# Kernel tuning notes

Measured on AMD Instinct MI355X. Metric: run time of the kernel, lower is better.

The kernel has to match this reference:

```python
import jax, jax.numpy as jnp
import numpy as np

EPS = 1e-7
MAX_NORM = 1.0 - 1e-3  # projection radius of the unit Poincare ball (c=1)
ALPHA = 0.2            # LeakyReLU negative slope
NEG_INF = -9e15


def _proj(x, max_norm=MAX_NORM):
    # Project points back inside the Poincare ball along the last dim.
    norm = jnp.clip(jnp.linalg.norm(x, axis=-1, keepdims=True), EPS)
    return jnp.where(norm > max_norm, x / norm * max_norm, x)


def _logmap0(x):
    # Log map at the origin of the Poincare ball, c = 1.
    norm = jnp.clip(jnp.linalg.norm(x, axis=-1, keepdims=True), EPS, 1.0 - EPS)
    return jnp.arctanh(norm) * x / norm


def _expmap0(v):
    # Exp map at the origin of the Poincare ball, c = 1.
    norm = jnp.clip(jnp.linalg.norm(v, axis=-1, keepdims=True), EPS)
    return jnp.tanh(norm) * v / norm


def setup_inputs() -> dict:
    key = jax.random.key(0)
    k1, k2, k3 = jax.random.split(key, 3)
    N, D = 12288, 128
    # points strictly inside the ball: ||x|| ~ 0.01*sqrt(128) ~ 0.11 < 1
    x = jax.random.normal(k1, (N, D), dtype=jnp.float32) * 0.01
    adj = jax.random.randint(k2, (N, N), 0, 2, dtype=jnp.int32)
    # attention vector a, as in init: N(0, 0.2) then proj(a, 0.9) row-wise
    a = jax.random.normal(k3, (2 * D, 1), dtype=jnp.float32) * 0.2
    a = _proj(a, 0.9)
    return {"x": x, "adj": adj, "a": a}


def reference(x, adj, a):
    D = a.shape[0] // 2
    x_tan = _logmap0(x)                       # [N, D]
    wh1 = x_tan @ a[:D]                       # [N, 1]
    wh2 = x_tan @ a[D:]                       # [N, 1]
    e = jax.nn.leaky_relu(wh1 + wh2.T, ALPHA)  # [N, N] additive scores
    scores = jnp.where(adj > 0, e, NEG_INF)
    attention = jax.nn.softmax(scores, axis=1)  # dropout omitted (eval mode)
    x_tan_prime = attention @ x_tan            # [N, D]
    return _proj(_expmap0(x_tan_prime))
```

## Files before the change

kernel.cpp:

```cpp
#include <hip/hip_runtime.h>
#include <math.h>

#define NN 12288
#define DD 128
#define EPSF 1e-7f
#define MAXNORM (1.0f - 1e-3f)
#define CSPLIT 4
#define CCOLS (NN / CSPLIT)
#define CSTEPS (CCOLS / 128)

typedef __attribute__((ext_vector_type(8))) short short8_t;
typedef __attribute__((ext_vector_type(4))) float float4_t;
typedef unsigned short ushort_t;

__device__ __forceinline__ unsigned short f2bf(float f) {
    unsigned int u = __builtin_bit_cast(unsigned int, f);
    unsigned int r = u + 0x7FFFu + ((u >> 16) & 1u);
    return (unsigned short)(r >> 16);
}

__global__ __launch_bounds__(128) void prep_kernel(
    const float* __restrict__ x, const float* __restrict__ a,
    ushort_t* __restrict__ xtb,
    float* __restrict__ wh1, float* __restrict__ wh2)
{
    const int r = blockIdx.x;
    const int t = threadIdx.x;
    const float xv = x[r * DD + t];
    const float a1 = a[t];
    const float a2 = a[DD + t];
    float s0 = xv * xv, s1 = xv * a1, s2 = xv * a2;
    #pragma unroll
    for (int o = 32; o > 0; o >>= 1) {
        s0 += __shfl_xor(s0, o);
        s1 += __shfl_xor(s1, o);
        s2 += __shfl_xor(s2, o);
    }
    __shared__ float red[6];
    const int w = t >> 6;
    if ((t & 63) == 0) { red[w * 3 + 0] = s0; red[w * 3 + 1] = s1; red[w * 3 + 2] = s2; }
    __syncthreads();
    const float sumsq = red[0] + red[3];
    const float d1    = red[1] + red[4];
    const float d2    = red[2] + red[5];
    const float nraw  = sqrtf(sumsq);
    const float nrm   = fminf(fmaxf(nraw, EPSF), 1.0f - EPSF);
    const float scale = atanhf(nrm) / nrm;
    xtb[(size_t)r * DD + t] = f2bf(xv * scale);
    if (t == 0) {
        wh1[r] = scale * d1;
        wh2[r] = scale * d2;
    }
}

__global__ __launch_bounds__(256) void swizzle_kernel(
    const ushort_t* __restrict__ xtb, ushort_t* __restrict__ xtB)
{
    __shared__ ushort_t raw[32 * 136];
    const int C = blockIdx.x;
    const int t = threadIdx.x;
    #pragma unroll
    for (int p = 0; p < 2; ++p) {
        const int idx = p * 256 + t;
        const int j = idx >> 4, cell = idx & 15;
        const uint4 v = *(const uint4*)(xtb + (size_t)(C * 32 + j) * DD + cell * 8);
        *(uint4*)&raw[j * 136 + cell * 8] = v;
    }
    __syncthreads();
    #pragma unroll
    for (int p = 0; p < 2; ++p) {
        const int oc = p * 256 + t;
        const int dt = oc >> 6;
        const int l6 = oc & 63;
        const int l15 = l6 & 15, q = l6 >> 4;
        short8_t v;
        #pragma unroll
        for (int e = 0; e < 8; ++e)
            v[e] = (short)raw[(q * 8 + e) * 136 + dt * 16 + l15];
        *(short8_t*)(xtB + (size_t)C * 4096 + oc * 8) = v;
    }
}

__global__ __launch_bounds__(256, 2) void attn_kernel(
    const int* __restrict__ adj,
    const ushort_t* __restrict__ xtB,
    const float* __restrict__ wh1, const float* __restrict__ wh2,
    float* __restrict__ pout, float* __restrict__ plsum)
{
    __shared__ __align__(16) ushort_t Bl0[128 * DD];
    __shared__ __align__(16) ushort_t Bl1[128 * DD];
    __shared__ __align__(16) float wh2_lds[CCOLS];

    const int t = threadIdx.x;
    const int w = t >> 6, lane = t & 63;
    const int l15 = lane & 15, quad = lane >> 4;
    const int cy = blockIdx.y;
    const int jcol0 = cy * CCOLS;
    const int rowbase = blockIdx.x * 64 + w * 16;

    #pragma unroll
    for (int m = 0; m < CCOLS / 256; ++m)
        wh2_lds[m * 256 + t] = wh2[jcol0 + m * 256 + t];
    const float wh1i = wh1[rowbase + l15];

    const int* adj_lane = adj + (size_t)(rowbase + l15) * NN + jcol0 + quad * 8;
    const uint4* Bsrc = (const uint4*)(xtB + (size_t)(jcol0 >> 5) * 4096);

    float4_t acc[8];
    #pragma unroll
    for (int dt = 0; dt < 8; ++dt) acc[dt] = (float4_t)0.0f;
    float lsum = 0.0f;

    uint4 sr[8];
    int4 Aa[8], Ab[8];

    auto stage_load = [&](int st) {
        const uint4* sp = Bsrc + (size_t)st * 2048 + t;
        #pragma unroll
        for (int r = 0; r < 8; ++r) sr[r] = sp[r * 256];
    };
    auto stage_write = [&](ushort_t* buf) {
        uint4* d = (uint4*)buf + t;
        #pragma unroll
        for (int r = 0; r < 8; ++r) d[r * 256] = sr[r];
    };
    auto adj_load = [&](int st, int4 (&A)[8]) {
        const int* bp = adj_lane + st * 128;
        #pragma unroll
        for (int kc = 0; kc < 4; ++kc) {
            A[kc * 2 + 0] = *(const int4*)(bp + kc * 32);
            A[kc * 2 + 1] = *(const int4*)(bp + kc * 32 + 4);
        }
    };

    auto compute = [&](int st, const ushort_t* buf, const int4 (&A)[8]) {
        #pragma unroll
        for (int kc = 0; kc < 4; ++kc) {
            const int4 Av = A[kc * 2 + 0], Ac = A[kc * 2 + 1];
            const int wbase = st * 128 + kc * 32 + quad * 8;
            const float4 Wa = *(const float4*)&wh2_lds[wbase];
            const float4 Wb = *(const float4*)&wh2_lds[wbase + 4];
            const float u0 = wh1i + Wa.x, u1 = wh1i + Wa.y;
            const float u2 = wh1i + Wa.z, u3 = wh1i + Wa.w;
            const float u4 = wh1i + Wb.x, u5 = wh1i + Wb.y;
            const float u6 = wh1i + Wb.z, u7 = wh1i + Wb.w;
            const float p0 = (Av.x > 0) ? __expf(fmaxf(u0, 0.2f * u0)) : 0.0f;
            const float p1 = (Av.y > 0) ? __expf(fmaxf(u1, 0.2f * u1)) : 0.0f;
            const float p2 = (Av.z > 0) ? __expf(fmaxf(u2, 0.2f * u2)) : 0.0f;
            const float p3 = (Av.w > 0) ? __expf(fmaxf(u3, 0.2f * u3)) : 0.0f;
            const float p4 = (Ac.x > 0) ? __expf(fmaxf(u4, 0.2f * u4)) : 0.0f;
            const float p5 = (Ac.y > 0) ? __expf(fmaxf(u5, 0.2f * u5)) : 0.0f;
            const float p6 = (Ac.z > 0) ? __expf(fmaxf(u6, 0.2f * u6)) : 0.0f;
            const float p7 = (Ac.w > 0) ? __expf(fmaxf(u7, 0.2f * u7)) : 0.0f;
            lsum += ((p0 + p1) + (p2 + p3)) + ((p4 + p5) + (p6 + p7));
            short8_t af;
            af[0] = (short)f2bf(p0); af[1] = (short)f2bf(p1);
            af[2] = (short)f2bf(p2); af[3] = (short)f2bf(p3);
            af[4] = (short)f2bf(p4); af[5] = (short)f2bf(p5);
            af[6] = (short)f2bf(p6); af[7] = (short)f2bf(p7);
            const ushort_t* Bp = buf + kc * 4096 + lane * 8;
            #pragma unroll
            for (int dt = 0; dt < 8; ++dt) {
                const short8_t Bf = *(const short8_t*)(Bp + dt * 512);
                acc[dt] = __builtin_amdgcn_mfma_f32_16x16x32_bf16(af, Bf, acc[dt], 0, 0, 0);
            }
        }
    };

    stage_load(0);
    stage_write(Bl0);
    adj_load(0, Aa);
    __syncthreads();

    #pragma unroll 1
    for (int st0 = 0; st0 < CSTEPS; st0 += 2) {
        if (st0 + 1 < CSTEPS) { stage_load(st0 + 1); adj_load(st0 + 1, Ab); }
        compute(st0, Bl0, Aa);
        if (st0 + 1 < CSTEPS) stage_write(Bl1);
        __syncthreads();
        if (st0 + 1 >= CSTEPS) break;
        if (st0 + 2 < CSTEPS) { stage_load(st0 + 2); adj_load(st0 + 2, Aa); }
        compute(st0 + 1, Bl1, Ab);
        if (st0 + 2 < CSTEPS) stage_write(Bl0);
        __syncthreads();
    }

    float v = lsum;
    v += __shfl_xor(v, 16);
    v += __shfl_xor(v, 32);
    if (quad == 0) plsum[(size_t)cy * NN + rowbase + l15] = v;
    #pragma unroll
    for (int dt = 0; dt < 8; ++dt)
        #pragma unroll
        for (int reg = 0; reg < 4; ++reg)
            pout[((size_t)cy * NN + rowbase + quad * 4 + reg) * DD + dt * 16 + l15]
                = acc[dt][reg];
}

__global__ __launch_bounds__(128) void reduce_kernel(
    const float* __restrict__ pout, const float* __restrict__ plsum,
    float* __restrict__ out)
{
    const int i = blockIdx.x;
    const int t = threadIdx.x;
    float v = 0.0f;
    #pragma unroll
    for (int s = 0; s < CSPLIT; ++s) v += pout[((size_t)s * NN + i) * DD + t];
    float ls = 0.0f;
    #pragma unroll
    for (int s = 0; s < CSPLIT; ++s) ls += plsum[(size_t)s * NN + i];
    v /= ls;
    float ss = v * v;
    #pragma unroll
    for (int o = 1; o < 64; o <<= 1) ss += __shfl_xor(ss, o);
    __shared__ float r2[2];
    if ((t & 63) == 0) r2[t >> 6] = ss;
    __syncthreads();
    const float total = r2[0] + r2[1];
    const float nraw = sqrtf(total);
    const float nv   = fmaxf(nraw, EPSF);
    const float th   = tanhf(nv);
    const float ysc  = th / nv;
    const float nyr  = ysc * nraw;
    const float ny   = fmaxf(nyr, EPSF);
    const float psc  = (ny > MAXNORM) ? (MAXNORM / ny) : 1.0f;
    const float os   = ysc * psc;
    out[(size_t)i * DD + t] = v * os;
}

extern "C" void kernel_launch(void* const* d_in, const int* in_sizes, int n_in,
                              void* d_out, int out_size, void* d_ws, size_t ws_size,
                              hipStream_t stream) {
    const float* x   = (const float*)d_in[0];
    const int*   adj = (const int*)d_in[1];
    const float* a   = (const float*)d_in[2];
    float* out = (float*)d_out;

    char* ws = (char*)d_ws;
    ushort_t* xtb = (ushort_t*)ws;  ws += (size_t)NN * DD * sizeof(ushort_t);
    ushort_t* xtB = (ushort_t*)ws;  ws += (size_t)NN * DD * sizeof(ushort_t);
    float* wh1 = (float*)ws;        ws += NN * sizeof(float);
    float* wh2 = (float*)ws;        ws += NN * sizeof(float);
    float* plsum = (float*)ws;      ws += (size_t)CSPLIT * NN * sizeof(float);
    float* pout  = (float*)ws;

    prep_kernel<<<NN, 128, 0, stream>>>(x, a, xtb, wh1, wh2);
    swizzle_kernel<<<NN / 32, 256, 0, stream>>>(xtb, xtB);
    attn_kernel<<<dim3(NN / 64, CSPLIT), 256, 0, stream>>>(
        adj, xtB, wh1, wh2, pout, plsum);
    reduce_kernel<<<NN, 128, 0, stream>>>(pout, plsum, out);
}
```

Before: 951.4 us.

## Stage B tiles in 512-row slabs and triple-buffer adjacency loads

The attention kernel drops its double-buffered 128-row LDS stages and instead loads a 512-row slab of bf16 features into one 128 KB shared buffer. Each slab then feeds four compute steps with only two barriers per slab. Adjacency rows are now prefetched two steps ahead through three register buffers, with the loop fully unrolled so the buffer choice is resolved at compile time. The aim is fewer barriers and longer-latency hiding for the adjacency stream. In exchange, occupancy drops to one block per CU (launch bounds go from 2 to 1), and the slab load is no longer overlapped with compute, so each slab stalls on the full copy.

```diff
diff --git a/kernel.cpp b/kernel.cpp
--- a/kernel.cpp
+++ b/kernel.cpp
@@ -8,6 +8,7 @@
 #define CSPLIT 4
 #define CCOLS (NN / CSPLIT)
 #define CSTEPS (CCOLS / 128)
+#define SLABS (CSTEPS / 4)
 
 typedef __attribute__((ext_vector_type(8))) short short8_t;
 typedef __attribute__((ext_vector_type(4))) float float4_t;
@@ -81,14 +82,13 @@
     }
 }
 
-__global__ __launch_bounds__(256, 2) void attn_kernel(
+__global__ __launch_bounds__(256, 1) void attn_kernel(
     const int* __restrict__ adj,
     const ushort_t* __restrict__ xtB,
     const float* __restrict__ wh1, const float* __restrict__ wh2,
     float* __restrict__ pout, float* __restrict__ plsum)
 {
-    __shared__ __align__(16) ushort_t Bl0[128 * DD];
-    __shared__ __align__(16) ushort_t Bl1[128 * DD];
+    __shared__ __align__(16) ushort_t B_lds[512 * DD];
     __shared__ __align__(16) float wh2_lds[CCOLS];
 
     const int t = threadIdx.x;
@@ -111,19 +111,8 @@
     for (int dt = 0; dt < 8; ++dt) acc[dt] = (float4_t)0.0f;
     float lsum = 0.0f;
 
-    uint4 sr[8];
-    int4 Aa[8], Ab[8];
-
-    auto stage_load = [&](int st) {
-        const uint4* sp = Bsrc + (size_t)st * 2048 + t;
-        #pragma unroll
-        for (int r = 0; r < 8; ++r) sr[r] = sp[r * 256];
-    };
-    auto stage_write = [&](ushort_t* buf) {
-        uint4* d = (uint4*)buf + t;
-        #pragma unroll
-        for (int r = 0; r < 8; ++r) d[r * 256] = sr[r];
-    };
+    int4 A0[8], A1[8], A2[8];
+
     auto adj_load = [&](int st, int4 (&A)[8]) {
         const int* bp = adj_lane + st * 128;
         #pragma unroll
@@ -133,7 +122,29 @@
         }
     };
 
-    auto compute = [&](int st, const ushort_t* buf, const int4 (&A)[8]) {
+    auto stage = [&](int sl) {
+        const uint4* sp = Bsrc + (size_t)sl * 8192 + t;
+        uint4* d = (uint4*)B_lds + t;
+        uint4 sa[8], sb[8];
+        #pragma unroll
+        for (int m = 0; m < 8; ++m) sa[m] = sp[m * 256];
+        #pragma unroll
+        for (int m = 0; m < 8; ++m) sb[m] = sp[(8 + m) * 256];
+        #pragma unroll
+        for (int m = 0; m < 8; ++m) d[m * 256] = sa[m];
+        #pragma unroll
+        for (int m = 0; m < 8; ++m) sa[m] = sp[(16 + m) * 256];
+        #pragma unroll
+        for (int m = 0; m < 8; ++m) d[(8 + m) * 256] = sb[m];
+        #pragma unroll
+        for (int m = 0; m < 8; ++m) sb[m] = sp[(24 + m) * 256];
+        #pragma unroll
+        for (int m = 0; m < 8; ++m) d[(16 + m) * 256] = sa[m];
+        #pragma unroll
+        for (int m = 0; m < 8; ++m) d[(24 + m) * 256] = sb[m];
+    };
+
+    auto compute = [&](int st, const int4 (&A)[8]) {
         #pragma unroll
         for (int kc = 0; kc < 4; ++kc) {
             const int4 Av = A[kc * 2 + 0], Ac = A[kc * 2 + 1];
@@ -158,7 +169,7 @@
             af[2] = (short)f2bf(p2); af[3] = (short)f2bf(p3);
             af[4] = (short)f2bf(p4); af[5] = (short)f2bf(p5);
             af[6] = (short)f2bf(p6); af[7] = (short)f2bf(p7);
-            const ushort_t* Bp = buf + kc * 4096 + lane * 8;
+            const ushort_t* Bp = B_lds + ((st & 3) * 4 + kc) * 4096 + lane * 8;
             #pragma unroll
             for (int dt = 0; dt < 8; ++dt) {
                 const short8_t Bf = *(const short8_t*)(Bp + dt * 512);
@@ -167,22 +178,30 @@
         }
     };
 
-    stage_load(0);
-    stage_write(Bl0);
-    adj_load(0, Aa);
-    __syncthreads();
-
-    #pragma unroll 1
-    for (int st0 = 0; st0 < CSTEPS; st0 += 2) {
-        if (st0 + 1 < CSTEPS) { stage_load(st0 + 1); adj_load(st0 + 1, Ab); }
-        compute(st0, Bl0, Aa);
-        if (st0 + 1 < CSTEPS) stage_write(Bl1);
-        __syncthreads();
-        if (st0 + 1 >= CSTEPS) break;
-        if (st0 + 2 < CSTEPS) { stage_load(st0 + 2); adj_load(st0 + 2, Aa); }
-        compute(st0 + 1, Bl1, Ab);
-        if (st0 + 2 < CSTEPS) stage_write(Bl0);
-        __syncthreads();
+    adj_load(0, A0);
+    adj_load(1, A1);
+    stage(0);
+    __syncthreads();
+
+    #pragma unroll
+    for (int sl = 0; sl < SLABS; ++sl) {
+        if (sl > 0) {
+            __syncthreads();
+            stage(sl);
+            __syncthreads();
+        }
+        #pragma unroll
+        for (int q = 0; q < 4; ++q) {
+            const int st = sl * 4 + q;
+            if (st + 2 < CSTEPS) {
+                if (((st + 2) % 3) == 0)      adj_load(st + 2, A0);
+                else if (((st + 2) % 3) == 1) adj_load(st + 2, A1);
+                else                          adj_load(st + 2, A2);
+            }
+            if ((st % 3) == 0)      compute(st, A0);
+            else if ((st % 3) == 1) compute(st, A1);
+            else                    compute(st, A2);
+        }
     }
 
     float v = lsum;
```

Result: slower. 1.198 ms (+25.9%).
